# Kernel optimization log

Measured on AMD Instinct MI355X. Metric: run time of the kernel, lower is better.

## Reference

```python
import jax, jax.numpy as jnp
from jax import lax
import numpy as np

D = 256        # input_size / hidden_dim
NRELS = 8      # rel_types hard-coded in WeightedGNN
V = 50257      # ntokens
PAD = 0        # padding_idx
L = 64         # max sequence length
B = 16         # batch size


def layer_norm(x, eps=1e-5):
    # F.layer_norm with no affine params
    m = jnp.mean(x, axis=-1, keepdims=True)
    v = jnp.var(x, axis=-1, keepdims=True)
    return (x - m) * lax.rsqrt(v + eps)


def setup_inputs() -> dict:
    key = jax.random.key(0)
    ks = jax.random.split(key, 10)
    tokens = jax.random.randint(ks[0], (L, B), 0, V)            # [L, B] like torch input
    A_rels = jax.random.uniform(ks[1], (B, L, L, NRELS), dtype=jnp.float32)
    root = jax.random.uniform(ks[2], (B, L), dtype=jnp.float32)
    s = 1.0 / np.sqrt(D)
    emb_sem = (jax.random.normal(ks[3], (V, D), jnp.float32) * 0.02).at[PAD].set(0.0)
    W_proj_nbrs = jax.random.normal(ks[4], (D, NRELS * D), jnp.float32) * s
    b_proj_nbrs = jnp.zeros((NRELS * D,), jnp.float32)
    W_in = jax.random.normal(ks[5], (D, 3 * D), jnp.float32) * s
    b_in = jnp.zeros((3 * D,), jnp.float32)
    W_out = jax.random.normal(ks[6], (D, D), jnp.float32) * s
    b_out = jnp.zeros((D,), jnp.float32)
    return dict(tokens=tokens, A_rels=A_rels, root=root, emb_sem=emb_sem,
                W_proj_nbrs=W_proj_nbrs, b_proj_nbrs=b_proj_nbrs,
                W_in=W_in, b_in=b_in, W_out=W_out, b_out=b_out)


def reference(tokens, A_rels, root, emb_sem, W_proj_nbrs, b_proj_nbrs, W_in, b_in, W_out, b_out):
    tok = tokens.T                                  # [B, L]
    mask = tok != PAD                               # [B, L]
    lengths = mask.sum(axis=1)                      # [B]
    X_sem = emb_sem[tok]                            # [B, L, D] (pad row is zero)

    # in_proj(x) is identical every iteration (dropout is eval-mode identity) -> hoist
    shift, scale, proj_x = jnp.split(X_sem @ W_in + b_in, 3, axis=-1)  # each [B, L, D]

    def step(h_prev, i):
        # relation-typed neighbor projection + per-relation layer norm
        p = (h_prev @ W_proj_nbrs + b_proj_nbrs).reshape(B, L, NRELS, D)
        p = layer_norm(p)
        # weighted aggregation over source nodes i and relation types h
        lin_sum = jnp.einsum('bijh,bihd->bjd', A_rels, p)          # [B, L, D]
        shr = lin_sum - jnp.tanh(lin_sum)                          # shrink()
        h = jax.nn.relu(shift * layer_norm(proj_x + shr) + scale)  # gated update
        y = jnp.tanh(h @ W_out + b_out)
        y = jnp.where((i > lengths)[:, None, None], 0.0, y)        # masked_fill
        return y, None

    prev0 = jnp.zeros_like(X_sem)
    prev_level, _ = lax.scan(step, prev0, jnp.arange(L, 0, -1))    # i = L..1
    final_state = jnp.einsum('bih,bi->bh', prev_level, root)       # [B, D]
    return final_state
```

## Files before the change

### kernel.cpp

```cpp
#include <hip/hip_runtime.h>
#include <hip/hip_bf16.h>


#define DD 256
#define LLEN 64
#define BBAT 16
#define NROWS 1024

typedef __attribute__((ext_vector_type(8))) short short8;
typedef __attribute__((ext_vector_type(4))) float f32x4;

__device__ inline unsigned short f2bf(float x) {
    unsigned int u = __float_as_uint(x);
    unsigned int r = (u + 0x7fffu + ((u >> 16) & 1u)) >> 16;
    return (unsigned short)r;
}

__global__ void k_setup(const int* __restrict__ tokens, int* __restrict__ lengths) {
    int b = threadIdx.x;
    if (b < BBAT) {
        int c = 0;
        for (int l = 0; l < LLEN; ++l) c += (tokens[l * BBAT + b] != 0) ? 1 : 0;
        lengths[b] = c;
    }
}

__global__ __launch_bounds__(256) void k_cvtW(const float* __restrict__ Wp,
                                              unsigned short* __restrict__ Wf) {
    int t = blockIdx.x * 256 + threadIdx.x;
    int l = t & 63; int rest = t >> 6;
    int tk = rest & 7; rest >>= 3;
    int tn = rest & 15; int hh = rest >> 4;
    int kbase = tk * 32 + (l >> 4) * 8;
    int n = hh * 256 + tn * 16 + (l & 15);
    union { short8 v; unsigned short u[8]; } pk;
#pragma unroll
    for (int j = 0; j < 8; ++j) pk.u[j] = f2bf(Wp[(kbase + j) * 2048 + n]);
    *(short8*)(Wf + (long)t * 8) = pk.v;
}

__global__ __launch_bounds__(256) void k_cvtA(const float* __restrict__ A,
                                              unsigned short* __restrict__ Af) {
    int t = blockIdx.x * 256 + threadIdx.x;
    int lane = t & 63;
    int tk = (t >> 6) & 15;
    int jg = (t >> 10) & 3;
    int b  = t >> 12;
    int j = jg * 16 + (lane & 15);
    int kbase = tk * 32 + (lane >> 4) * 8;
    int h  = kbase >> 6;
    int i0 = kbase & 63;
    union { short8 v; unsigned short u[8]; } pk;
#pragma unroll
    for (int jj = 0; jj < 8; ++jj)
        pk.u[jj] = f2bf(A[((long)(b * 64 + i0 + jj) * 64 + j) * 8 + h]);
    *(short8*)(Af + (long)t * 8) = pk.v;
}

__global__ __launch_bounds__(256) void k_cvtWo(const float* __restrict__ Wo,
                                               unsigned short* __restrict__ Wof) {
    int t = blockIdx.x * 256 + threadIdx.x;
    int lane = t & 63;
    int tk = (t >> 6) & 7;
    int nt = t >> 9;
    int kbase = tk * 32 + (lane >> 4) * 8;
    int n = nt * 16 + (lane & 15);
    union { short8 v; unsigned short u[8]; } pk;
#pragma unroll
    for (int j = 0; j < 8; ++j) pk.u[j] = f2bf(Wo[(kbase + j) * 256 + n]);
    *(short8*)(Wof + (long)t * 8) = pk.v;
}

__global__ __launch_bounds__(256) void k_inproj(
    const int* __restrict__ tokens, const float* __restrict__ emb,
    const float* __restrict__ W_in, const float* __restrict__ b_in,
    float* __restrict__ shiftb, float* __restrict__ scaleb, float* __restrict__ projx)
{
    __shared__ float xs[8][DD];
    const int t = threadIdx.x;
    const int row0 = blockIdx.x * 8;
    for (int r = 0; r < 8; ++r) {
        int row = row0 + r;
        int b = row >> 6, l = row & 63;
        int tok = tokens[l * BBAT + b];
        xs[r][t] = emb[(long)tok * DD + t];
    }
    __syncthreads();
    float a0[8], a1[8], a2[8];
#pragma unroll
    for (int r = 0; r < 8; ++r) { a0[r] = a1[r] = a2[r] = 0.f; }
    for (int k = 0; k < DD; ++k) {
        float w0 = W_in[k * 768 + t];
        float w1 = W_in[k * 768 + 256 + t];
        float w2 = W_in[k * 768 + 512 + t];
#pragma unroll
        for (int r = 0; r < 8; ++r) {
            float x = xs[r][k];
            a0[r] = fmaf(x, w0, a0[r]);
            a1[r] = fmaf(x, w1, a1[r]);
            a2[r] = fmaf(x, w2, a2[r]);
        }
    }
    float bi0 = b_in[t], bi1 = b_in[256 + t], bi2 = b_in[512 + t];
#pragma unroll
    for (int r = 0; r < 8; ++r) {
        int row = row0 + r;
        shiftb[row * DD + t] = a0[r] + bi0;
        scaleb[row * DD + t] = a1[r] + bi1;
        projx [row * DD + t] = a2[r] + bi2;
    }
}

__global__ __launch_bounds__(256, 2) void k_proj(
    const unsigned short* __restrict__ h_bf,
    const unsigned short* __restrict__ Wf,
    const float* __restrict__ bp,
    unsigned short* __restrict__ Pf)
{
    __shared__ float Cs[16][260];
    __shared__ float part[4][16][2];
    const int t = threadIdx.x;
    const int wv = t >> 6, lane = t & 63;
    const int lin = blockIdx.x;
    const int xcd = lin & 7, q = lin >> 3;
    const int b = xcd + 8 * (q & 1);
    const int rest = q >> 1;
    const int hh = rest & 7;
    const int ig = rest >> 3;
    const int row0 = b * 64 + ig * 16;

    f32x4 acc[4];
#pragma unroll
    for (int tn = 0; tn < 4; ++tn) acc[tn] = (f32x4){0.f, 0.f, 0.f, 0.f};

    const unsigned short* aRow = h_bf + (row0 + (lane & 15)) * DD + (lane >> 4) * 8;
    const unsigned short* wBase = Wf + ((long)(hh * 16 + wv * 4) * 8) * 512 + lane * 8;
    short8 a8[8];
#pragma unroll
    for (int tk = 0; tk < 8; ++tk) a8[tk] = *(const short8*)(aRow + tk * 32);
#pragma unroll
    for (int tk = 0; tk < 8; ++tk) {
#pragma unroll
        for (int tn = 0; tn < 4; ++tn) {
            short8 bb = *(const short8*)(wBase + (long)(tn * 8 + tk) * 512);
            acc[tn] = __builtin_amdgcn_mfma_f32_16x16x32_bf16(a8[tk], bb, acc[tn], 0, 0, 0);
        }
    }
#pragma unroll
    for (int tn = 0; tn < 4; ++tn) {
        int n = wv * 64 + tn * 16 + (lane & 15);
        int m0 = (lane >> 4) * 4;
#pragma unroll
        for (int r = 0; r < 4; ++r) Cs[m0 + r][n] = acc[tn][r];
    }
    __syncthreads();
    const float bias = bp[hh * 256 + t];
    float vals[16];
#pragma unroll
    for (int r = 0; r < 16; ++r) vals[r] = Cs[r][t] + bias;
    for (int r = 0; r < 16; ++r) {
        float s = vals[r], ss = vals[r] * vals[r];
#pragma unroll
        for (int m = 32; m >= 1; m >>= 1) { s += __shfl_xor(s, m); ss += __shfl_xor(ss, m); }
        if (lane == 0) { part[wv][r][0] = s; part[wv][r][1] = ss; }
    }
    __syncthreads();
    float normed[16];
#pragma unroll
    for (int r = 0; r < 16; ++r) {
        float s  = part[0][r][0] + part[1][r][0] + part[2][r][0] + part[3][r][0];
        float ss = part[0][r][1] + part[1][r][1] + part[2][r][1] + part[3][r][1];
        float mean = s * (1.f / 256.f);
        float var  = ss * (1.f / 256.f) - mean * mean;
        float rstd = rsqrtf(var + 1e-5f);
        normed[r] = (vals[r] - mean) * rstd;
    }
    const int ibase = ig * 16;
#pragma unroll
    for (int g = 0; g < 2; ++g) {
        int k0 = hh * 64 + ibase + g * 8;
        int tk1 = k0 >> 5;
        int lane_s = ((k0 >> 3) & 3) * 16 + (t & 15);
        long off = (long)b * 131072 + tk1 * 8192 + (t >> 4) * 512 + lane_s * 8;
        union { short8 v; unsigned short u[8]; } pk;
#pragma unroll
        for (int jj = 0; jj < 8; ++jj) pk.u[jj] = f2bf(normed[g * 8 + jj]);
        *(short8*)(Pf + off) = pk.v;
    }
}

__global__ __launch_bounds__(1024) void k_agg(
    const unsigned short* __restrict__ Af,
    const unsigned short* __restrict__ Pf,
    const float* __restrict__ projx,
    const float* __restrict__ shiftb,
    const float* __restrict__ scaleb,
    const unsigned short* __restrict__ Wof,
    const float* __restrict__ bout,
    const int* __restrict__ lengths,
    float* __restrict__ h_out,
    unsigned short* __restrict__ h_bf,
    int i_val, int write_f32)
{
    __shared__ float Cs[16][260];
    __shared__ unsigned short hsb[16][264];
    __shared__ float part[16][4][2];
    const int t = threadIdx.x;
    const int w = t >> 6, lane = t & 63;
    const int b = blockIdx.x, jg = blockIdx.y;
    const int j0 = jg * 16;

    const unsigned short* ab = Af + ((long)(b * 4 + jg) * 16) * 512 + lane * 8;
    const unsigned short* pb = Pf + (long)b * 131072 + w * 512 + lane * 8;
    short8 bfr[16];
#pragma unroll
    for (int tk = 0; tk < 16; ++tk)
        bfr[tk] = *(const short8*)(pb + (long)tk * 8192);
    f32x4 acc = (f32x4){0.f, 0.f, 0.f, 0.f};
#pragma unroll
    for (int tk = 0; tk < 16; ++tk) {
        short8 a = *(const short8*)(ab + (long)tk * 512);
        acc = __builtin_amdgcn_mfma_f32_16x16x32_bf16(a, bfr[tk], acc, 0, 0, 0);
    }
    {
        int n = w * 16 + (lane & 15);
        int m0 = (lane >> 4) * 4;
#pragma unroll
        for (int r = 0; r < 4; ++r) Cs[m0 + r][n] = acc[r];
    }
    __syncthreads();

    const int d = t & 255;
    const int rbase = (w >> 2) * 4;
    const int dseg = w & 3;
    float tv[4];
#pragma unroll
    for (int ri = 0; ri < 4; ++ri) {
        int row = b * 64 + j0 + rbase + ri;
        float lin = Cs[rbase + ri][d];
        float shr = lin - tanhf(lin);
        tv[ri] = projx[row * DD + d] + shr;
    }
#pragma unroll
    for (int ri = 0; ri < 4; ++ri) {
        float s = tv[ri], ss = tv[ri] * tv[ri];
#pragma unroll
        for (int m = 32; m >= 1; m >>= 1) { s += __shfl_xor(s, m); ss += __shfl_xor(ss, m); }
        if (lane == 0) { part[rbase + ri][dseg][0] = s; part[rbase + ri][dseg][1] = ss; }
    }
    __syncthreads();
#pragma unroll
    for (int ri = 0; ri < 4; ++ri) {
        int r = rbase + ri;
        int row = b * 64 + j0 + r;
        float s  = part[r][0][0] + part[r][1][0] + part[r][2][0] + part[r][3][0];
        float ss = part[r][0][1] + part[r][1][1] + part[r][2][1] + part[r][3][1];
        float mean = s * (1.f / 256.f);
        float var  = ss * (1.f / 256.f) - mean * mean;
        float rstd = rsqrtf(var + 1e-5f);
        float nv = (tv[ri] - mean) * rstd;
        float hv = fmaf(shiftb[row * DD + d], nv, scaleb[row * DD + d]);
        hsb[r][d] = f2bf(fmaxf(hv, 0.f));
    }
    __syncthreads();

    f32x4 acc2 = (f32x4){0.f, 0.f, 0.f, 0.f};
#pragma unroll
    for (int tk = 0; tk < 8; ++tk) {
        short8 a = *(const short8*)(&hsb[lane & 15][tk * 32 + (lane >> 4) * 8]);
        short8 wf = *(const short8*)(Wof + (long)(w * 8 + tk) * 512 + lane * 8);
        acc2 = __builtin_amdgcn_mfma_f32_16x16x32_bf16(a, wf, acc2, 0, 0, 0);
    }
    {
        int n = w * 16 + (lane & 15);
        int m0 = (lane >> 4) * 4;
#pragma unroll
        for (int r = 0; r < 4; ++r) Cs[m0 + r][n] = acc2[r];
    }
    __syncthreads();
    const float bo_d = bout[d];
    const bool maskz = (i_val > lengths[b]);
#pragma unroll
    for (int ri = 0; ri < 4; ++ri) {
        int r = rbase + ri;
        int row = b * 64 + j0 + r;
        float y = tanhf(Cs[r][d] + bo_d);
        float ym = maskz ? 0.f : y;
        h_bf[row * DD + d] = f2bf(ym);
        if (write_f32) h_out[row * DD + d] = ym;
    }
}

__global__ __launch_bounds__(256) void k_final(
    const float* __restrict__ h_buf, const float* __restrict__ root,
    float* __restrict__ out)
{
    const int t = threadIdx.x;
    const int b = blockIdx.x;
    float acc = 0.f;
    for (int i = 0; i < LLEN; ++i)
        acc = fmaf(h_buf[(b * 64 + i) * DD + t], root[b * 64 + i], acc);
    out[b * DD + t] = acc;
}

extern "C" void kernel_launch(void* const* d_in, const int* in_sizes, int n_in,
                              void* d_out, int out_size, void* d_ws, size_t ws_size,
                              hipStream_t stream)
{
    const int*   tokens = (const int*)  d_in[0];
    const float* A      = (const float*)d_in[1];
    const float* root   = (const float*)d_in[2];
    const float* emb    = (const float*)d_in[3];
    const float* Wp     = (const float*)d_in[4];
    const float* bp     = (const float*)d_in[5];
    const float* Wi     = (const float*)d_in[6];
    const float* bi     = (const float*)d_in[7];
    const float* Wo     = (const float*)d_in[8];
    const float* bo     = (const float*)d_in[9];
    float* out = (float*)d_out;

    char* ws = (char*)d_ws;
    int*   lengths = (int*)(ws + 0);
    float* shiftb  = (float*)(ws + 1024);
    float* scaleb  = shiftb + NROWS * DD;
    float* projx   = scaleb + NROWS * DD;
    float* h_out   = projx  + NROWS * DD;
    unsigned short* h_bf = (unsigned short*)(h_out + NROWS * DD);
    unsigned short* Wf   = h_bf + NROWS * DD;
    unsigned short* Pf   = Wf + 524288;
    unsigned short* Af   = Pf + 2097152;
    unsigned short* Wof  = Af + 524288;

    hipMemsetAsync(h_bf, 0, (size_t)NROWS * DD * sizeof(unsigned short), stream);
    k_setup<<<1, 64, 0, stream>>>(tokens, lengths);
    k_cvtW<<<256, 256, 0, stream>>>(Wp, Wf);
    k_cvtA<<<256, 256, 0, stream>>>(A, Af);
    k_cvtWo<<<32, 256, 0, stream>>>(Wo, Wof);
    k_inproj<<<128, 256, 0, stream>>>(tokens, emb, Wi, bi, shiftb, scaleb, projx);
    for (int it = 0; it < 64; ++it) {
        int i_val = 64 - it;
        k_proj<<<512, 256, 0, stream>>>(h_bf, Wf, bp, Pf);
        k_agg<<<dim3(16, 4), 1024, 0, stream>>>(Af, Pf, projx, shiftb, scaleb,
                                                Wof, bo, lengths, h_out, h_bf,
                                                i_val, (it == 63) ? 1 : 0);
    }
    k_final<<<16, 256, 0, stream>>>(h_out, root, out);
}
```

Before: 1.567 ms.

## Fuse recurrent loop into one cooperative persistent kernel with per-batch barriers

Replaces the 128 per-step kernel launches (projection + aggregation for 64 iterations) with a single cooperative persistent kernel of 128 blocks. Each batch gets 8 blocks that synchronise through a per-batch atomic generation barrier in global memory. The setup, conversion and in-projection kernels are merged into one prep launch, and the final root reduction is folded into the loop kernel. This removes launch overhead and inter-kernel gaps, but adds spin-barrier costs and idles half of the blocks during the aggregation phase.

```diff
diff --git a/kernel.cpp b/kernel.cpp
--- a/kernel.cpp
+++ b/kernel.cpp
@@ -16,291 +16,308 @@
     return (unsigned short)r;
 }
 
-__global__ void k_setup(const int* __restrict__ tokens, int* __restrict__ lengths) {
-    int b = threadIdx.x;
-    if (b < BBAT) {
-        int c = 0;
-        for (int l = 0; l < LLEN; ++l) c += (tokens[l * BBAT + b] != 0) ? 1 : 0;
-        lengths[b] = c;
+__device__ inline void batch_bar(int* ctr, int* gen) {
+    __syncthreads();
+    if (threadIdx.x == 0) {
+        int g = __hip_atomic_load(gen, __ATOMIC_RELAXED, __HIP_MEMORY_SCOPE_AGENT);
+        __threadfence();
+        int prev = __hip_atomic_fetch_add(ctr, 1, __ATOMIC_ACQ_REL, __HIP_MEMORY_SCOPE_AGENT);
+        if (prev == 7) {
+            __hip_atomic_store(ctr, 0, __ATOMIC_RELAXED, __HIP_MEMORY_SCOPE_AGENT);
+            __hip_atomic_store(gen, g + 1, __ATOMIC_RELEASE, __HIP_MEMORY_SCOPE_AGENT);
+        } else {
+            int spins = 0;
+            while (__hip_atomic_load(gen, __ATOMIC_RELAXED, __HIP_MEMORY_SCOPE_AGENT) == g) {
+                __builtin_amdgcn_s_sleep(1);
+                if (++spins > (1 << 24)) break;
+            }
+        }
+        __threadfence();
     }
-}
-
-__global__ __launch_bounds__(256) void k_cvtW(const float* __restrict__ Wp,
-                                              unsigned short* __restrict__ Wf) {
-    int t = blockIdx.x * 256 + threadIdx.x;
-    int l = t & 63; int rest = t >> 6;
-    int tk = rest & 7; rest >>= 3;
-    int tn = rest & 15; int hh = rest >> 4;
-    int kbase = tk * 32 + (l >> 4) * 8;
-    int n = hh * 256 + tn * 16 + (l & 15);
-    union { short8 v; unsigned short u[8]; } pk;
-#pragma unroll
-    for (int j = 0; j < 8; ++j) pk.u[j] = f2bf(Wp[(kbase + j) * 2048 + n]);
-    *(short8*)(Wf + (long)t * 8) = pk.v;
-}
-
-__global__ __launch_bounds__(256) void k_cvtA(const float* __restrict__ A,
-                                              unsigned short* __restrict__ Af) {
-    int t = blockIdx.x * 256 + threadIdx.x;
-    int lane = t & 63;
-    int tk = (t >> 6) & 15;
-    int jg = (t >> 10) & 3;
-    int b  = t >> 12;
-    int j = jg * 16 + (lane & 15);
-    int kbase = tk * 32 + (lane >> 4) * 8;
-    int h  = kbase >> 6;
-    int i0 = kbase & 63;
-    union { short8 v; unsigned short u[8]; } pk;
-#pragma unroll
-    for (int jj = 0; jj < 8; ++jj)
-        pk.u[jj] = f2bf(A[((long)(b * 64 + i0 + jj) * 64 + j) * 8 + h]);
-    *(short8*)(Af + (long)t * 8) = pk.v;
-}
-
-__global__ __launch_bounds__(256) void k_cvtWo(const float* __restrict__ Wo,
-                                               unsigned short* __restrict__ Wof) {
-    int t = blockIdx.x * 256 + threadIdx.x;
-    int lane = t & 63;
-    int tk = (t >> 6) & 7;
-    int nt = t >> 9;
-    int kbase = tk * 32 + (lane >> 4) * 8;
-    int n = nt * 16 + (lane & 15);
-    union { short8 v; unsigned short u[8]; } pk;
-#pragma unroll
-    for (int j = 0; j < 8; ++j) pk.u[j] = f2bf(Wo[(kbase + j) * 256 + n]);
-    *(short8*)(Wof + (long)t * 8) = pk.v;
-}
-
-__global__ __launch_bounds__(256) void k_inproj(
-    const int* __restrict__ tokens, const float* __restrict__ emb,
-    const float* __restrict__ W_in, const float* __restrict__ b_in,
-    float* __restrict__ shiftb, float* __restrict__ scaleb, float* __restrict__ projx)
+    __syncthreads();
+}
+
+__global__ __launch_bounds__(256) void k_prep(
+    const int* __restrict__ tokens, const float* __restrict__ A,
+    const float* __restrict__ emb,
+    const float* __restrict__ Wp, const float* __restrict__ Wi,
+    const float* __restrict__ bi, const float* __restrict__ Wo,
+    unsigned short* __restrict__ Wf, unsigned short* __restrict__ Af,
+    unsigned short* __restrict__ Wof,
+    float* __restrict__ shiftb, float* __restrict__ scaleb, float* __restrict__ projx,
+    int* __restrict__ lengths, int* __restrict__ bar)
 {
     __shared__ float xs[8][DD];
-    const int t = threadIdx.x;
-    const int row0 = blockIdx.x * 8;
-    for (int r = 0; r < 8; ++r) {
-        int row = row0 + r;
-        int b = row >> 6, l = row & 63;
-        int tok = tokens[l * BBAT + b];
-        xs[r][t] = emb[(long)tok * DD + t];
+    const int tid = threadIdx.x;
+    const int bid = blockIdx.x;
+
+    if (bid < 256) {
+        int t = bid * 256 + tid;
+        int l = t & 63; int rest = t >> 6;
+        int tk = rest & 7; rest >>= 3;
+        int tn = rest & 15; int hh = rest >> 4;
+        int kbase = tk * 32 + (l >> 4) * 8;
+        int n = hh * 256 + tn * 16 + (l & 15);
+        union { short8 v; unsigned short u[8]; } pk;
+#pragma unroll
+        for (int j = 0; j < 8; ++j) pk.u[j] = f2bf(Wp[(kbase + j) * 2048 + n]);
+        *(short8*)(Wf + (long)t * 8) = pk.v;
+    } else if (bid < 512) {
+        int t = (bid - 256) * 256 + tid;
+        int lane = t & 63;
+        int tk = (t >> 6) & 15;
+        int jg = (t >> 10) & 3;
+        int b  = t >> 12;
+        int j = jg * 16 + (lane & 15);
+        int kbase = tk * 32 + (lane >> 4) * 8;
+        int h  = kbase >> 6;
+        int i0 = kbase & 63;
+        union { short8 v; unsigned short u[8]; } pk;
+#pragma unroll
+        for (int jj = 0; jj < 8; ++jj)
+            pk.u[jj] = f2bf(A[((long)(b * 64 + i0 + jj) * 64 + j) * 8 + h]);
+        *(short8*)(Af + (long)t * 8) = pk.v;
+    } else if (bid < 544) {
+        int t = (bid - 512) * 256 + tid;
+        int lane = t & 63;
+        int tk = (t >> 6) & 7;
+        int nt = t >> 9;
+        int kbase = tk * 32 + (lane >> 4) * 8;
+        int n = nt * 16 + (lane & 15);
+        union { short8 v; unsigned short u[8]; } pk;
+#pragma unroll
+        for (int j = 0; j < 8; ++j) pk.u[j] = f2bf(Wo[(kbase + j) * 256 + n]);
+        *(short8*)(Wof + (long)t * 8) = pk.v;
+    } else if (bid < 928) {
+        int lb = bid - 544;
+        int rowx = lb & 127, nc = lb >> 7;
+        const int row0 = rowx * 8;
+        for (int r = 0; r < 8; ++r) {
+            int row = row0 + r;
+            int b = row >> 6, l = row & 63;
+            int tok = tokens[l * BBAT + b];
+            xs[r][tid] = emb[(long)tok * DD + tid];
+        }
+        __syncthreads();
+        const int col = nc * 256 + tid;
+        float a[8];
+#pragma unroll
+        for (int r = 0; r < 8; ++r) a[r] = 0.f;
+#pragma unroll 4
+        for (int k = 0; k < DD; ++k) {
+            float wv = Wi[k * 768 + col];
+#pragma unroll
+            for (int r = 0; r < 8; ++r) a[r] = fmaf(xs[r][k], wv, a[r]);
+        }
+        const float bia = bi[col];
+        float* dst = (nc == 0) ? shiftb : (nc == 1) ? scaleb : projx;
+#pragma unroll
+        for (int r = 0; r < 8; ++r) dst[(row0 + r) * DD + tid] = a[r] + bia;
+    } else {
+        if (tid < 32) bar[tid] = 0;
+        if (tid < BBAT) {
+            int c = 0;
+            for (int l = 0; l < LLEN; ++l) c += (tokens[l * BBAT + tid] != 0) ? 1 : 0;
+            lengths[tid] = c;
+        }
     }
-    __syncthreads();
-    float a0[8], a1[8], a2[8];
-#pragma unroll
-    for (int r = 0; r < 8; ++r) { a0[r] = a1[r] = a2[r] = 0.f; }
-    for (int k = 0; k < DD; ++k) {
-        float w0 = W_in[k * 768 + t];
-        float w1 = W_in[k * 768 + 256 + t];
-        float w2 = W_in[k * 768 + 512 + t];
-#pragma unroll
-        for (int r = 0; r < 8; ++r) {
-            float x = xs[r][k];
-            a0[r] = fmaf(x, w0, a0[r]);
-            a1[r] = fmaf(x, w1, a1[r]);
-            a2[r] = fmaf(x, w2, a2[r]);
-        }
-    }
-    float bi0 = b_in[t], bi1 = b_in[256 + t], bi2 = b_in[512 + t];
-#pragma unroll
-    for (int r = 0; r < 8; ++r) {
-        int row = row0 + r;
-        shiftb[row * DD + t] = a0[r] + bi0;
-        scaleb[row * DD + t] = a1[r] + bi1;
-        projx [row * DD + t] = a2[r] + bi2;
-    }
-}
-
-__global__ __launch_bounds__(256, 2) void k_proj(
-    const unsigned short* __restrict__ h_bf,
-    const unsigned short* __restrict__ Wf,
-    const float* __restrict__ bp,
-    unsigned short* __restrict__ Pf)
-{
-    __shared__ float Cs[16][260];
-    __shared__ float part[4][16][2];
-    const int t = threadIdx.x;
-    const int wv = t >> 6, lane = t & 63;
-    const int lin = blockIdx.x;
-    const int xcd = lin & 7, q = lin >> 3;
-    const int b = xcd + 8 * (q & 1);
-    const int rest = q >> 1;
-    const int hh = rest & 7;
-    const int ig = rest >> 3;
-    const int row0 = b * 64 + ig * 16;
-
-    f32x4 acc[4];
-#pragma unroll
-    for (int tn = 0; tn < 4; ++tn) acc[tn] = (f32x4){0.f, 0.f, 0.f, 0.f};
-
-    const unsigned short* aRow = h_bf + (row0 + (lane & 15)) * DD + (lane >> 4) * 8;
-    const unsigned short* wBase = Wf + ((long)(hh * 16 + wv * 4) * 8) * 512 + lane * 8;
-    short8 a8[8];
-#pragma unroll
-    for (int tk = 0; tk < 8; ++tk) a8[tk] = *(const short8*)(aRow + tk * 32);
-#pragma unroll
-    for (int tk = 0; tk < 8; ++tk) {
-#pragma unroll
-        for (int tn = 0; tn < 4; ++tn) {
-            short8 bb = *(const short8*)(wBase + (long)(tn * 8 + tk) * 512);
-            acc[tn] = __builtin_amdgcn_mfma_f32_16x16x32_bf16(a8[tk], bb, acc[tn], 0, 0, 0);
-        }
-    }
-#pragma unroll
-    for (int tn = 0; tn < 4; ++tn) {
-        int n = wv * 64 + tn * 16 + (lane & 15);
-        int m0 = (lane >> 4) * 4;
-#pragma unroll
-        for (int r = 0; r < 4; ++r) Cs[m0 + r][n] = acc[tn][r];
-    }
-    __syncthreads();
-    const float bias = bp[hh * 256 + t];
-    float vals[16];
-#pragma unroll
-    for (int r = 0; r < 16; ++r) vals[r] = Cs[r][t] + bias;
-    for (int r = 0; r < 16; ++r) {
-        float s = vals[r], ss = vals[r] * vals[r];
-#pragma unroll
-        for (int m = 32; m >= 1; m >>= 1) { s += __shfl_xor(s, m); ss += __shfl_xor(ss, m); }
-        if (lane == 0) { part[wv][r][0] = s; part[wv][r][1] = ss; }
-    }
-    __syncthreads();
-    float normed[16];
-#pragma unroll
-    for (int r = 0; r < 16; ++r) {
-        float s  = part[0][r][0] + part[1][r][0] + part[2][r][0] + part[3][r][0];
-        float ss = part[0][r][1] + part[1][r][1] + part[2][r][1] + part[3][r][1];
-        float mean = s * (1.f / 256.f);
-        float var  = ss * (1.f / 256.f) - mean * mean;
-        float rstd = rsqrtf(var + 1e-5f);
-        normed[r] = (vals[r] - mean) * rstd;
-    }
-    const int ibase = ig * 16;
-#pragma unroll
-    for (int g = 0; g < 2; ++g) {
-        int k0 = hh * 64 + ibase + g * 8;
-        int tk1 = k0 >> 5;
-        int lane_s = ((k0 >> 3) & 3) * 16 + (t & 15);
-        long off = (long)b * 131072 + tk1 * 8192 + (t >> 4) * 512 + lane_s * 8;
-        union { short8 v; unsigned short u[8]; } pk;
-#pragma unroll
-        for (int jj = 0; jj < 8; ++jj) pk.u[jj] = f2bf(normed[g * 8 + jj]);
-        *(short8*)(Pf + off) = pk.v;
-    }
-}
-
-__global__ __launch_bounds__(1024) void k_agg(
+}
+
+__global__ __launch_bounds__(1024) void k_loop(
     const unsigned short* __restrict__ Af,
-    const unsigned short* __restrict__ Pf,
+    unsigned short* __restrict__ Pf,
     const float* __restrict__ projx,
     const float* __restrict__ shiftb,
     const float* __restrict__ scaleb,
+    const unsigned short* __restrict__ Wf,
+    const float* __restrict__ bp,
     const unsigned short* __restrict__ Wof,
     const float* __restrict__ bout,
     const int* __restrict__ lengths,
     float* __restrict__ h_out,
     unsigned short* __restrict__ h_bf,
-    int i_val, int write_f32)
+    const float* __restrict__ root,
+    float* __restrict__ out,
+    int* __restrict__ bar)
 {
-    __shared__ float Cs[16][260];
+    __shared__ float Cs4[4][16][260];
+    __shared__ float part4[4][4][16][2];
+    __shared__ float CsA[16][260];
     __shared__ unsigned short hsb[16][264];
-    __shared__ float part[16][4][2];
+    __shared__ float partA[16][4][2];
+
     const int t = threadIdx.x;
     const int w = t >> 6, lane = t & 63;
-    const int b = blockIdx.x, jg = blockIdx.y;
-    const int j0 = jg * 16;
-
-    const unsigned short* ab = Af + ((long)(b * 4 + jg) * 16) * 512 + lane * 8;
-    const unsigned short* pb = Pf + (long)b * 131072 + w * 512 + lane * 8;
-    short8 bfr[16];
-#pragma unroll
-    for (int tk = 0; tk < 16; ++tk)
-        bfr[tk] = *(const short8*)(pb + (long)tk * 8192);
-    f32x4 acc = (f32x4){0.f, 0.f, 0.f, 0.f};
-#pragma unroll
-    for (int tk = 0; tk < 16; ++tk) {
-        short8 a = *(const short8*)(ab + (long)tk * 512);
-        acc = __builtin_amdgcn_mfma_f32_16x16x32_bf16(a, bfr[tk], acc, 0, 0, 0);
-    }
-    {
-        int n = w * 16 + (lane & 15);
-        int m0 = (lane >> 4) * 4;
-#pragma unroll
-        for (int r = 0; r < 4; ++r) Cs[m0 + r][n] = acc[r];
-    }
-    __syncthreads();
-
+    const int bid = blockIdx.x;
+    const int t2 = bid >> 3;
+    const int q = t2 & 7;
+    const int b = (bid & 7) + 8 * (t2 >> 3);
+    const int hh = q;
+    int* ctr = bar + b * 2;
+    int* gen = bar + b * 2 + 1;
+    const int len_b = lengths[b];
+
+    const int ig = w >> 2, wv = w & 3;
+    const int row0 = b * 64 + ig * 16;
+    const unsigned short* aRow = h_bf + (row0 + (lane & 15)) * DD + (lane >> 4) * 8;
+    const unsigned short* wBase = Wf + ((long)(hh * 16 + wv * 4) * 8) * 512 + lane * 8;
+    const int g2 = t >> 8;
+    const int tc = t & 255;
+    const float biasP = bp[hh * 256 + tc];
     const int d = t & 255;
     const int rbase = (w >> 2) * 4;
     const int dseg = w & 3;
-    float tv[4];
-#pragma unroll
-    for (int ri = 0; ri < 4; ++ri) {
-        int row = b * 64 + j0 + rbase + ri;
-        float lin = Cs[rbase + ri][d];
-        float shr = lin - tanhf(lin);
-        tv[ri] = projx[row * DD + d] + shr;
+    const float bo_d = bout[d];
+
+    for (int it = 0; it < 64; ++it) {
+        {
+            f32x4 acc[4];
+#pragma unroll
+            for (int tn = 0; tn < 4; ++tn) acc[tn] = (f32x4){0.f, 0.f, 0.f, 0.f};
+            short8 a8[8];
+#pragma unroll
+            for (int tk = 0; tk < 8; ++tk) a8[tk] = *(const short8*)(aRow + tk * 32);
+#pragma unroll
+            for (int tk = 0; tk < 8; ++tk) {
+#pragma unroll
+                for (int tn = 0; tn < 4; ++tn) {
+                    short8 bbv = *(const short8*)(wBase + (long)(tn * 8 + tk) * 512);
+                    acc[tn] = __builtin_amdgcn_mfma_f32_16x16x32_bf16(a8[tk], bbv, acc[tn], 0, 0, 0);
+                }
+            }
+#pragma unroll
+            for (int tn = 0; tn < 4; ++tn) {
+                int n = wv * 64 + tn * 16 + (lane & 15);
+                int m0 = (lane >> 4) * 4;
+#pragma unroll
+                for (int r = 0; r < 4; ++r) Cs4[ig][m0 + r][n] = acc[tn][r];
+            }
+        }
+        __syncthreads();
+        {
+            float vals[16];
+#pragma unroll
+            for (int r = 0; r < 16; ++r) vals[r] = Cs4[g2][r][tc] + biasP;
+            for (int r = 0; r < 16; ++r) {
+                float s = vals[r], ss = vals[r] * vals[r];
+#pragma unroll
+                for (int m = 32; m >= 1; m >>= 1) { s += __shfl_xor(s, m); ss += __shfl_xor(ss, m); }
+                if (lane == 0) { part4[g2][wv][r][0] = s; part4[g2][wv][r][1] = ss; }
+            }
+            __syncthreads();
+            float normed[16];
+#pragma unroll
+            for (int r = 0; r < 16; ++r) {
+                float s  = part4[g2][0][r][0] + part4[g2][1][r][0] + part4[g2][2][r][0] + part4[g2][3][r][0];
+                float ss = part4[g2][0][r][1] + part4[g2][1][r][1] + part4[g2][2][r][1] + part4[g2][3][r][1];
+                float mean = s * (1.f / 256.f);
+                float var  = ss * (1.f / 256.f) - mean * mean;
+                float rstd = rsqrtf(var + 1e-5f);
+                normed[r] = (vals[r] - mean) * rstd;
+            }
+            const int ibase = g2 * 16;
+#pragma unroll
+            for (int g = 0; g < 2; ++g) {
+                int k0 = hh * 64 + ibase + g * 8;
+                int tk1 = k0 >> 5;
+                int lane_s = ((k0 >> 3) & 3) * 16 + (tc & 15);
+                long off = (long)b * 131072 + tk1 * 8192 + (tc >> 4) * 512 + lane_s * 8;
+                union { short8 v; unsigned short u[8]; } pk;
+#pragma unroll
+                for (int jj = 0; jj < 8; ++jj) pk.u[jj] = f2bf(normed[g * 8 + jj]);
+                *(short8*)(Pf + off) = pk.v;
+            }
+        }
+        batch_bar(ctr, gen);
+
+        if (q < 4) {
+            const int jg = q;
+            const unsigned short* ab = Af + ((long)(b * 4 + jg) * 16) * 512 + lane * 8;
+            const unsigned short* pb = Pf + (long)b * 131072 + w * 512 + lane * 8;
+            short8 bfr[16];
+#pragma unroll
+            for (int tk = 0; tk < 16; ++tk)
+                bfr[tk] = *(const short8*)(pb + (long)tk * 8192);
+            f32x4 acc = (f32x4){0.f, 0.f, 0.f, 0.f};
+#pragma unroll
+            for (int tk = 0; tk < 16; ++tk) {
+                short8 a = *(const short8*)(ab + (long)tk * 512);
+                acc = __builtin_amdgcn_mfma_f32_16x16x32_bf16(a, bfr[tk], acc, 0, 0, 0);
+            }
+            {
+                int n = w * 16 + (lane & 15);
+                int m0 = (lane >> 4) * 4;
+#pragma unroll
+                for (int r = 0; r < 4; ++r) CsA[m0 + r][n] = acc[r];
+            }
+            __syncthreads();
+
+            float tv[4];
+#pragma unroll
+            for (int ri = 0; ri < 4; ++ri) {
+                int row = b * 64 + jg * 16 + rbase + ri;
+                float lin = CsA[rbase + ri][d];
+                float shr = lin - tanhf(lin);
+                tv[ri] = projx[row * DD + d] + shr;
+            }
+#pragma unroll
+            for (int ri = 0; ri < 4; ++ri) {
+                float s = tv[ri], ss = tv[ri] * tv[ri];
+#pragma unroll
+                for (int m = 32; m >= 1; m >>= 1) { s += __shfl_xor(s, m); ss += __shfl_xor(ss, m); }
+                if (lane == 0) { partA[rbase + ri][dseg][0] = s; partA[rbase + ri][dseg][1] = ss; }
+            }
+            __syncthreads();
+#pragma unroll
+            for (int ri = 0; ri < 4; ++ri) {
+                int r = rbase + ri;
+                int row = b * 64 + jg * 16 + r;
+                float s  = partA[r][0][0] + partA[r][1][0] + partA[r][2][0] + partA[r][3][0];
+                float ss = partA[r][0][1] + partA[r][1][1] + partA[r][2][1] + partA[r][3][1];
+                float mean = s * (1.f / 256.f);
+                float var  = ss * (1.f / 256.f) - mean * mean;
+                float rstd = rsqrtf(var + 1e-5f);
+                float nv = (tv[ri] - mean) * rstd;
+                float hv = fmaf(shiftb[row * DD + d], nv, scaleb[row * DD + d]);
+                hsb[r][d] = f2bf(fmaxf(hv, 0.f));
+            }
+            __syncthreads();
+
+            f32x4 acc2 = (f32x4){0.f, 0.f, 0.f, 0.f};
+#pragma unroll
+            for (int tk = 0; tk < 8; ++tk) {
+                short8 a = *(const short8*)(&hsb[lane & 15][tk * 32 + (lane >> 4) * 8]);
+                short8 wf = *(const short8*)(Wof + (long)(w * 8 + tk) * 512 + lane * 8);
+                acc2 = __builtin_amdgcn_mfma_f32_16x16x32_bf16(a, wf, acc2, 0, 0, 0);
+            }
+            {
+                int n = w * 16 + (lane & 15);
+                int m0 = (lane >> 4) * 4;
+#pragma unroll
+                for (int r = 0; r < 4; ++r) CsA[m0 + r][n] = acc2[r];
+            }
+            __syncthreads();
+            const int i_val = 64 - it;
+            const bool maskz = (i_val > len_b);
+#pragma unroll
+            for (int ri = 0; ri < 4; ++ri) {
+                int r = rbase + ri;
+                int row = b * 64 + jg * 16 + r;
+                float y = tanhf(CsA[r][d] + bo_d);
+                float ym = maskz ? 0.f : y;
+                h_bf[row * DD + d] = f2bf(ym);
+                if (it == 63) h_out[row * DD + d] = ym;
+            }
+        }
+        batch_bar(ctr, gen);
     }
-#pragma unroll
-    for (int ri = 0; ri < 4; ++ri) {
-        float s = tv[ri], ss = tv[ri] * tv[ri];
-#pragma unroll
-        for (int m = 32; m >= 1; m >>= 1) { s += __shfl_xor(s, m); ss += __shfl_xor(ss, m); }
-        if (lane == 0) { part[rbase + ri][dseg][0] = s; part[rbase + ri][dseg][1] = ss; }
+
+    if (q == 0 && t < DD) {
+        float accf = 0.f;
+        for (int i = 0; i < LLEN; ++i)
+            accf = fmaf(h_out[(b * 64 + i) * DD + t], root[b * 64 + i], accf);
+        out[b * DD + t] = accf;
     }
-    __syncthreads();
-#pragma unroll
-    for (int ri = 0; ri < 4; ++ri) {
-        int r = rbase + ri;
-        int row = b * 64 + j0 + r;
-        float s  = part[r][0][0] + part[r][1][0] + part[r][2][0] + part[r][3][0];
-        float ss = part[r][0][1] + part[r][1][1] + part[r][2][1] + part[r][3][1];
-        float mean = s * (1.f / 256.f);
-        float var  = ss * (1.f / 256.f) - mean * mean;
-        float rstd = rsqrtf(var + 1e-5f);
-        float nv = (tv[ri] - mean) * rstd;
-        float hv = fmaf(shiftb[row * DD + d], nv, scaleb[row * DD + d]);
-        hsb[r][d] = f2bf(fmaxf(hv, 0.f));
-    }
-    __syncthreads();
-
-    f32x4 acc2 = (f32x4){0.f, 0.f, 0.f, 0.f};
-#pragma unroll
-    for (int tk = 0; tk < 8; ++tk) {
-        short8 a = *(const short8*)(&hsb[lane & 15][tk * 32 + (lane >> 4) * 8]);
-        short8 wf = *(const short8*)(Wof + (long)(w * 8 + tk) * 512 + lane * 8);
-        acc2 = __builtin_amdgcn_mfma_f32_16x16x32_bf16(a, wf, acc2, 0, 0, 0);
-    }
-    {
-        int n = w * 16 + (lane & 15);
-        int m0 = (lane >> 4) * 4;
-#pragma unroll
-        for (int r = 0; r < 4; ++r) Cs[m0 + r][n] = acc2[r];
-    }
-    __syncthreads();
-    const float bo_d = bout[d];
-    const bool maskz = (i_val > lengths[b]);
-#pragma unroll
-    for (int ri = 0; ri < 4; ++ri) {
-        int r = rbase + ri;
-        int row = b * 64 + j0 + r;
-        float y = tanhf(Cs[r][d] + bo_d);
-        float ym = maskz ? 0.f : y;
-        h_bf[row * DD + d] = f2bf(ym);
-        if (write_f32) h_out[row * DD + d] = ym;
-    }
-}
-
-__global__ __launch_bounds__(256) void k_final(
-    const float* __restrict__ h_buf, const float* __restrict__ root,
-    float* __restrict__ out)
-{
-    const int t = threadIdx.x;
-    const int b = blockIdx.x;
-    float acc = 0.f;
-    for (int i = 0; i < LLEN; ++i)
-        acc = fmaf(h_buf[(b * 64 + i) * DD + t], root[b * 64 + i], acc);
-    out[b * DD + t] = acc;
 }
 
 extern "C" void kernel_launch(void* const* d_in, const int* in_sizes, int n_in,
@@ -321,6 +338,7 @@
 
     char* ws = (char*)d_ws;
     int*   lengths = (int*)(ws + 0);
+    int*   bar     = (int*)(ws + 256);
     float* shiftb  = (float*)(ws + 1024);
     float* scaleb  = shiftb + NROWS * DD;
     float* projx   = scaleb + NROWS * DD;
@@ -332,17 +350,10 @@
     unsigned short* Wof  = Af + 524288;
 
     hipMemsetAsync(h_bf, 0, (size_t)NROWS * DD * sizeof(unsigned short), stream);
-    k_setup<<<1, 64, 0, stream>>>(tokens, lengths);
-    k_cvtW<<<256, 256, 0, stream>>>(Wp, Wf);
-    k_cvtA<<<256, 256, 0, stream>>>(A, Af);
-    k_cvtWo<<<32, 256, 0, stream>>>(Wo, Wof);
-    k_inproj<<<128, 256, 0, stream>>>(tokens, emb, Wi, bi, shiftb, scaleb, projx);
-    for (int it = 0; it < 64; ++it) {
-        int i_val = 64 - it;
-        k_proj<<<512, 256, 0, stream>>>(h_bf, Wf, bp, Pf);
-        k_agg<<<dim3(16, 4), 1024, 0, stream>>>(Af, Pf, projx, shiftb, scaleb,
-                                                Wof, bo, lengths, h_out, h_bf,
-                                                i_val, (it == 63) ? 1 : 0);
-    }
-    k_final<<<16, 256, 0, stream>>>(h_out, root, out);
-}
+    k_prep<<<929, 256, 0, stream>>>(tokens, A, emb, Wp, Wi, bi, Wo,
+                                    Wf, Af, Wof, shiftb, scaleb, projx, lengths, bar);
+    void* kargs[] = { (void*)&Af, (void*)&Pf, (void*)&projx, (void*)&shiftb, (void*)&scaleb,
+                      (void*)&Wf, (void*)&bp, (void*)&Wof, (void*)&bo, (void*)&lengths,
+                      (void*)&h_out, (void*)&h_bf, (void*)&root, (void*)&out, (void*)&bar };
+    hipLaunchCooperativeKernel((const void*)k_loop, dim3(128), dim3(1024), kargs, 0, stream);
+}
```

Result: slower. 5.138 ms (+227.8%).
